# Kernel tuning notes

Measured on AMD Instinct MI355X. Metric: run time of the kernel, lower is better.

Reference implementation:

```python
import jax, jax.numpy as jnp
import numpy as np

IN_F, OUT_F = 4096, 16384
ACT_IN, ACT_OUT = 2048, 8192
B, S = 4, 2048


def setup_inputs() -> dict:
    key = jax.random.key(0)
    k1, k2, k3 = jax.random.split(key, 3)
    rng = np.random.default_rng(0)
    in_idx = jnp.asarray(np.sort(rng.choice(IN_F, size=ACT_IN, replace=False)), dtype=jnp.int32)
    out_idx = jnp.asarray(np.sort(rng.choice(OUT_F, size=ACT_OUT, replace=False)), dtype=jnp.int32)
    x = jax.random.normal(k1, (B, S, IN_F), dtype=jnp.float32)
    # nn.Linear init scale ~ 1/sqrt(fan_in)
    weight = jax.random.normal(k2, (ACT_OUT, ACT_IN), dtype=jnp.float32) / np.sqrt(ACT_IN)
    bias = jax.random.normal(k3, (ACT_OUT,), dtype=jnp.float32) / np.sqrt(ACT_IN)
    return {"x": x, "weight": weight, "bias": bias, "in_indices": in_idx, "out_indices": out_idx}


def reference(x, weight, bias, in_indices, out_indices):
    batch_dims = x.shape[:-1]
    x_flat = x.reshape(-1, IN_F)                      # [N, in_f]
    x_active = x_flat[:, in_indices]                  # gather cols -> [N, act_in]
    y_active = jnp.einsum('ni,oi->no', x_active, weight) + bias  # [N, act_out]
    out_flat = jnp.zeros((x_flat.shape[0], OUT_F), dtype=y_active.dtype)
    out_flat = out_flat.at[:, out_indices].set(y_active)  # scatter cols
    return out_flat.reshape(batch_dims + (OUT_F,))
```

## Files before the change

### kernel.cpp

```cpp
#include <hip/hip_runtime.h>
#include <stdint.h>

#define IN_F    4096
#define OUT_F   16384
#define ACT_IN  2048
#define ACT_OUT 8192
#define NROWS   8192

typedef __bf16 bf16;
typedef __bf16 bf16x8 __attribute__((ext_vector_type(8)));
typedef float  f32x4  __attribute__((ext_vector_type(4)));

#define BM 128
#define BN 128
#define BK 32
#define TSTRIDE 34
#define CMAX 64

__device__ __forceinline__ void g2lds16(const void* g, void* l) {
  __builtin_amdgcn_global_load_lds(
      (const __attribute__((address_space(1))) void*)(uintptr_t)g,
      (__attribute__((address_space(3))) void*)(uint32_t)(uintptr_t)l,
      16, 0, 0);
}

__global__ void gather_cast_x(const float* __restrict__ x,
                              const int* __restrict__ in_idx,
                              bf16* __restrict__ A) {
  int n  = blockIdx.x;
  int k0 = threadIdx.x << 3;
  const float* xr = x + (size_t)n * IN_F;
  int4 i0 = *reinterpret_cast<const int4*>(in_idx + k0);
  int4 i1 = *reinterpret_cast<const int4*>(in_idx + k0 + 4);
  bf16x8 v;
  v[0] = (bf16)xr[i0.x]; v[1] = (bf16)xr[i0.y];
  v[2] = (bf16)xr[i0.z]; v[3] = (bf16)xr[i0.w];
  v[4] = (bf16)xr[i1.x]; v[5] = (bf16)xr[i1.y];
  v[6] = (bf16)xr[i1.z]; v[7] = (bf16)xr[i1.w];
  *reinterpret_cast<bf16x8*>(A + (size_t)n * ACT_IN + k0) = v;
}

__global__ void cast_w_kernel(const float* __restrict__ w, bf16* __restrict__ W) {
  size_t base = ((size_t)blockIdx.x * blockDim.x + threadIdx.x) * 8;
  float4 f0 = *reinterpret_cast<const float4*>(w + base);
  float4 f1 = *reinterpret_cast<const float4*>(w + base + 4);
  bf16x8 v;
  v[0] = (bf16)f0.x; v[1] = (bf16)f0.y; v[2] = (bf16)f0.z; v[3] = (bf16)f0.w;
  v[4] = (bf16)f1.x; v[5] = (bf16)f1.y; v[6] = (bf16)f1.z; v[7] = (bf16)f1.w;
  *reinterpret_cast<bf16x8*>(W + base) = v;
}

__global__ __launch_bounds__(256, 2)
void gemm_scatter(const bf16* __restrict__ A,
                  const bf16* __restrict__ W,
                  const float* __restrict__ bias,
                  const int* __restrict__ out_idx,
                  float* __restrict__ out) {
  __shared__ __align__(16) char smraw[128 * TSTRIDE * 4 + CMAX * 4];
  bf16* As = (bf16*)smraw;
  bf16* Bs = (bf16*)(smraw + BM * BK * 2);
  float* tile = (float*)smraw;
  int*   cmap = (int*)(smraw + 128 * TSTRIDE * 4);

  const int tid  = threadIdx.x;
  const int lane = tid & 63;
  const int quad = lane >> 4;
  const int l16  = lane & 15;
  const int wave = tid >> 6;
  const int wm   = (wave & 1) << 6;
  const int wn   = (wave >> 1) << 6;
  const int m0   = blockIdx.y * BM;
  const int n0   = blockIdx.x * BN;

  const int se   = tid << 3;
  const int srow = se >> 5;
  const int scol = se & 31;
  const bf16* Ag0 = A + (size_t)(m0 + srow) * ACT_IN + scol;
  const bf16* Ag1 = Ag0 + (size_t)64 * ACT_IN;
  const bf16* Bg0 = W + (size_t)(n0 + srow) * ACT_IN + scol;
  const bf16* Bg1 = Bg0 + (size_t)64 * ACT_IN;
  bf16* lA0 = As + se;
  bf16* lA1 = As + 64 * BK + se;
  bf16* lB0 = Bs + se;
  bf16* lB1 = Bs + 64 * BK + se;

  f32x4 acc[4][4] = {};

  for (int k0 = 0; k0 < ACT_IN; k0 += BK) {
    g2lds16(Ag0 + k0, lA0);
    g2lds16(Ag1 + k0, lA1);
    g2lds16(Bg0 + k0, lB0);
    g2lds16(Bg1 + k0, lB1);
    __syncthreads();

    bf16x8 af[4], bfr[4];
#pragma unroll
    for (int i = 0; i < 4; ++i)
      af[i] = *reinterpret_cast<const bf16x8*>(As + (wm + i * 16 + l16) * BK + quad * 8);
#pragma unroll
    for (int j = 0; j < 4; ++j)
      bfr[j] = *reinterpret_cast<const bf16x8*>(Bs + (wn + j * 16 + l16) * BK + quad * 8);

#pragma unroll
    for (int i = 0; i < 4; ++i)
#pragma unroll
      for (int j = 0; j < 4; ++j)
        acc[i][j] = __builtin_amdgcn_mfma_f32_16x16x32_bf16(af[i], bfr[j], acc[i][j], 0, 0, 0);

    __syncthreads();
  }

  for (int cc = 0; cc < 4; ++cc) {
    __syncthreads();
    if ((cc >> 1) == (wn >> 6)) {
#pragma unroll
      for (int jj = 0; jj < 2; ++jj) {
        const int j  = ((cc & 1) << 1) + jj;
        const int cl = (jj << 4) + l16;
        const float bv = bias[n0 + wn + j * 16 + l16];
#pragma unroll
        for (int i = 0; i < 4; ++i) {
          const int rb = wm + i * 16 + (quad << 2);
#pragma unroll
          for (int r = 0; r < 4; ++r)
            tile[(rb + r) * TSTRIDE + cl] = acc[i][j][r] + bv;
        }
      }
    }

    const int a0   = n0 + cc * 32;
    const int lo   = (a0 == 0) ? 0 : out_idx[a0 - 1] + 1;
    const int aend = out_idx[a0 + 31];
    const int hi   = (a0 + 31 == ACT_OUT - 1) ? OUT_F - 1 : aend;

    for (int base = lo; base <= hi; base += CMAX) {
      int wd = hi - base + 1; if (wd > CMAX) wd = CMAX;
      __syncthreads();
      if (tid < CMAX) cmap[tid] = -1;
      __syncthreads();
      if (tid < 32) {
        int rel = out_idx[a0 + tid] - base;
        if (rel >= 0 && rel < CMAX) cmap[rel] = tid;
      }
      __syncthreads();
      const int lc = tid & 63;
      if (lc < wd) {
        const int cm = cmap[lc];
        size_t ob = (size_t)(m0 + wave * 32) * OUT_F + base + lc;
#pragma unroll 4
        for (int r = 0; r < 32; ++r) {
          float v = (cm >= 0) ? tile[(wave * 32 + r) * TSTRIDE + cm] : 0.0f;
          out[ob + (size_t)r * OUT_F] = v;
        }
      }
    }
  }
}

extern "C" void kernel_launch(void* const* d_in, const int* in_sizes, int n_in,
                              void* d_out, int out_size, void* d_ws, size_t ws_size,
                              hipStream_t stream) {
  const float* x       = (const float*)d_in[0];
  const float* w       = (const float*)d_in[1];
  const float* bias    = (const float*)d_in[2];
  const int*   in_idx  = (const int*)d_in[3];
  const int*   out_idx = (const int*)d_in[4];
  float* out = (float*)d_out;

  bf16* A  = (bf16*)d_ws;
  bf16* Wb = (bf16*)((char*)d_ws + (size_t)NROWS * ACT_IN * 2);

  gather_cast_x<<<NROWS, 256, 0, stream>>>(x, in_idx, A);
  cast_w_kernel<<<(ACT_OUT * (size_t)ACT_IN / 8) / 256, 256, 0, stream>>>(w, Wb);
  gemm_scatter<<<dim3(ACT_OUT / BN, NROWS / BM), 256, 0, stream>>>(A, Wb, bias, out_idx, out);
}
```

Measured before the change: 1.020 ms.

## Enlarge GEMM tiles to 256x256 with a 4-stage async LDS pipeline and swizzle

```diff
diff --git a/kernel.cpp b/kernel.cpp
--- a/kernel.cpp
+++ b/kernel.cpp
@@ -11,9 +11,12 @@
 typedef __bf16 bf16x8 __attribute__((ext_vector_type(8)));
 typedef float  f32x4  __attribute__((ext_vector_type(4)));
 
-#define BM 128
-#define BN 128
+#define BM 256
+#define BN 256
 #define BK 32
+#define KSTEPS   (ACT_IN / BK)
+#define ABYTES   (BM * BK * 2)
+#define BUFBYTES (2 * ABYTES)
 #define TSTRIDE 34
 #define CMAX 64
 
@@ -23,6 +26,12 @@
       (__attribute__((address_space(3))) void*)(uint32_t)(uintptr_t)l,
       16, 0, 0);
 }
+
+#define WAITVM(n) do { asm volatile("s_waitcnt vmcnt(" #n ")" ::: "memory"); \
+                       __builtin_amdgcn_sched_barrier(0); } while (0)
+#define BARRIER() do { asm volatile("" ::: "memory");                        \
+                       __builtin_amdgcn_s_barrier();                         \
+                       asm volatile("" ::: "memory"); } while (0)
 
 __global__ void gather_cast_x(const float* __restrict__ x,
                               const int* __restrict__ in_idx,
@@ -50,76 +59,92 @@
   *reinterpret_cast<bf16x8*>(W + base) = v;
 }
 
-__global__ __launch_bounds__(256, 2)
+__global__ __launch_bounds__(512, 2)
 void gemm_scatter(const bf16* __restrict__ A,
                   const bf16* __restrict__ W,
                   const float* __restrict__ bias,
                   const int* __restrict__ out_idx,
                   float* __restrict__ out) {
-  __shared__ __align__(16) char smraw[128 * TSTRIDE * 4 + CMAX * 4];
-  bf16* As = (bf16*)smraw;
-  bf16* Bs = (bf16*)(smraw + BM * BK * 2);
-  float* tile = (float*)smraw;
-  int*   cmap = (int*)(smraw + 128 * TSTRIDE * 4);
+  __shared__ __align__(16) char smraw[4 * BUFBYTES];
 
   const int tid  = threadIdx.x;
   const int lane = tid & 63;
   const int quad = lane >> 4;
   const int l16  = lane & 15;
   const int wave = tid >> 6;
-  const int wm   = (wave & 1) << 6;
+  const int wm   = (wave & 1) << 7;
   const int wn   = (wave >> 1) << 6;
   const int m0   = blockIdx.y * BM;
   const int n0   = blockIdx.x * BN;
 
-  const int se   = tid << 3;
-  const int srow = se >> 5;
-  const int scol = se & 31;
-  const bf16* Ag0 = A + (size_t)(m0 + srow) * ACT_IN + scol;
-  const bf16* Ag1 = Ag0 + (size_t)64 * ACT_IN;
-  const bf16* Bg0 = W + (size_t)(n0 + srow) * ACT_IN + scol;
-  const bf16* Bg1 = Bg0 + (size_t)64 * ACT_IN;
-  bf16* lA0 = As + se;
-  bf16* lA1 = As + 64 * BK + se;
-  bf16* lB0 = Bs + se;
-  bf16* lB1 = Bs + 64 * BK + se;
-
-  f32x4 acc[4][4] = {};
-
-  for (int k0 = 0; k0 < ACT_IN; k0 += BK) {
-    g2lds16(Ag0 + k0, lA0);
-    g2lds16(Ag1 + k0, lA1);
-    g2lds16(Bg0 + k0, lB0);
-    g2lds16(Bg1 + k0, lB1);
+  const int srow = tid >> 2;
+  const int sq   = (tid & 3) ^ ((tid >> 4) & 3);
+  const bf16* Ag0 = A + (size_t)(m0 + srow) * ACT_IN + sq * 8;
+  const bf16* Ag1 = Ag0 + (size_t)128 * ACT_IN;
+  const bf16* Bg0 = W + (size_t)(n0 + srow) * ACT_IN + sq * 8;
+  const bf16* Bg1 = Bg0 + (size_t)128 * ACT_IN;
+  const int dA0 = tid * 16;
+  const int dA1 = 8192 + tid * 16;
+  const int dB0 = ABYTES + tid * 16;
+  const int dB1 = ABYTES + 8192 + tid * 16;
+
+  const int ksw  = (quad ^ ((l16 >> 2) & 3)) << 4;
+  const int aoff = (wm + l16) * 64 + ksw;
+  const int boff = ABYTES + (wn + l16) * 64 + ksw;
+
+  f32x4 acc[8][4] = {};
+
+#define ISSUE(s) do {                                                        \
+    char* sb_ = smraw + (((s) & 3) * BUFBYTES);                              \
+    const size_t ko_ = (size_t)(s) * BK;                                     \
+    g2lds16(Ag0 + ko_, sb_ + dA0);                                           \
+    g2lds16(Ag1 + ko_, sb_ + dA1);                                           \
+    g2lds16(Bg0 + ko_, sb_ + dB0);                                           \
+    g2lds16(Bg1 + ko_, sb_ + dB1);                                           \
+  } while (0)
+
+#define STEP(s, ISS, VMN) do {                                               \
+    const char* sb_ = smraw + (((s) & 3) * BUFBYTES);                        \
+    bf16x8 af[8], bfr[4];                                                    \
+    _Pragma("unroll") for (int i = 0; i < 8; ++i)                            \
+      af[i] = *reinterpret_cast<const bf16x8*>(sb_ + aoff + i * 1024);       \
+    _Pragma("unroll") for (int j = 0; j < 4; ++j)                            \
+      bfr[j] = *reinterpret_cast<const bf16x8*>(sb_ + boff + j * 1024);      \
+    if (ISS) ISSUE((s) + 3);                                                 \
+    __builtin_amdgcn_s_setprio(1);                                           \
+    _Pragma("unroll") for (int i = 0; i < 8; ++i)                            \
+      _Pragma("unroll") for (int j = 0; j < 4; ++j)                          \
+        acc[i][j] = __builtin_amdgcn_mfma_f32_16x16x32_bf16(af[i], bfr[j],   \
+                                                      acc[i][j], 0, 0, 0);   \
+    __builtin_amdgcn_s_setprio(0);                                           \
+    WAITVM(VMN);                                                             \
+    BARRIER();                                                               \
+  } while (0)
+
+  ISSUE(0); ISSUE(1); ISSUE(2);
+  WAITVM(8);
+  BARRIER();
+
+#pragma unroll 1
+  for (int s = 0; s < KSTEPS - 3; ++s) STEP(s, 1, 8);
+  STEP(KSTEPS - 3, 0, 4);
+  STEP(KSTEPS - 2, 0, 0);
+  STEP(KSTEPS - 1, 0, 0);
+
+  __syncthreads();
+  float* tile = (float*)smraw;
+  int*   cmap = (int*)(smraw + 256 * TSTRIDE * 4);
+
+  for (int cc = 0; cc < 8; ++cc) {
     __syncthreads();
-
-    bf16x8 af[4], bfr[4];
-#pragma unroll
-    for (int i = 0; i < 4; ++i)
-      af[i] = *reinterpret_cast<const bf16x8*>(As + (wm + i * 16 + l16) * BK + quad * 8);
-#pragma unroll
-    for (int j = 0; j < 4; ++j)
-      bfr[j] = *reinterpret_cast<const bf16x8*>(Bs + (wn + j * 16 + l16) * BK + quad * 8);
-
-#pragma unroll
-    for (int i = 0; i < 4; ++i)
-#pragma unroll
-      for (int j = 0; j < 4; ++j)
-        acc[i][j] = __builtin_amdgcn_mfma_f32_16x16x32_bf16(af[i], bfr[j], acc[i][j], 0, 0, 0);
-
-    __syncthreads();
-  }
-
-  for (int cc = 0; cc < 4; ++cc) {
-    __syncthreads();
-    if ((cc >> 1) == (wn >> 6)) {
+    if ((cc >> 1) == (wave >> 1)) {
 #pragma unroll
       for (int jj = 0; jj < 2; ++jj) {
         const int j  = ((cc & 1) << 1) + jj;
         const int cl = (jj << 4) + l16;
         const float bv = bias[n0 + wn + j * 16 + l16];
 #pragma unroll
-        for (int i = 0; i < 4; ++i) {
+        for (int i = 0; i < 8; ++i) {
           const int rb = wm + i * 16 + (quad << 2);
 #pragma unroll
           for (int r = 0; r < 4; ++r)
@@ -155,6 +180,8 @@
       }
     }
   }
+#undef STEP
+#undef ISSUE
 }
 
 extern "C" void kernel_launch(void* const* d_in, const int* in_sizes, int n_in,
@@ -172,5 +199,5 @@
 
   gather_cast_x<<<NROWS, 256, 0, stream>>>(x, in_idx, A);
   cast_w_kernel<<<(ACT_OUT * (size_t)ACT_IN / 8) / 256, 256, 0, stream>>>(w, Wb);
-  gemm_scatter<<<dim3(ACT_OUT / BN, NROWS / BM), 256, 0, stream>>>(A, Wb, bias, out_idx, out);
-}
+  gemm_scatter<<<dim3(ACT_OUT / BN, NROWS / BM), 512, 0, stream>>>(A, Wb, bias, out_idx, out);
+}
```

New measurement: 1.040 ms. No clear change (+2.0%).
